# Optimization experiments

Measured on AMD Instinct MI355X. Metric: run time of the kernel, lower is better.

The kernel has to match this reference:

```python
import jax, jax.numpy as jnp
import numpy as np

B, T, D, H = 4, 2048, 512, 8
DK = D // H

def setup_inputs() -> dict:
    key = jax.random.key(0)
    ks = jax.random.split(key, 5)
    s = 1.0 / np.sqrt(D)
    return {
        "x": jax.random.normal(ks[0], (B, T, D), dtype=jnp.float32),
        "Wq": jax.random.normal(ks[1], (D, D), dtype=jnp.float32) * s,
        "bq": jnp.zeros((D,), dtype=jnp.float32),
        "Wk": jax.random.normal(ks[2], (D, D), dtype=jnp.float32) * s,
        "bk": jnp.zeros((D,), dtype=jnp.float32),
        "Wv": jax.random.normal(ks[3], (D, D), dtype=jnp.float32) * s,
        "bv": jnp.zeros((D,), dtype=jnp.float32),
        "Wo": jax.random.normal(ks[4], (D, D), dtype=jnp.float32) * s,
        "bo": jnp.zeros((D,), dtype=jnp.float32),
    }

def reference(x, Wq, bq, Wk, bk, Wv, bv, Wo, bo):
    # Linear projections (torch Linear: x @ W.T + b); split into heads.
    q = (x @ Wq.T + bq).reshape(B, T, H, DK)  # [B,T,H,dk]
    k = (x @ Wk.T + bk).reshape(B, T, H, DK)
    v = (x @ Wv.T + bv).reshape(B, T, H, DK)
    scale = 1.0 / np.sqrt(DK)
    # scores: [B,H,T,T]
    scores = jnp.einsum("bqhd,bkhd->bhqk", q, k) * scale
    attn = jax.nn.softmax(scores, axis=-1)
    ctx = jnp.einsum("bhqk,bkhd->bqhd", attn, v).reshape(B, T, D)
    return ctx @ Wo.T + bo
```

## Files before the change

### kernel.cpp

```cpp
#include <hip/hip_runtime.h>
#include <stdint.h>

#define NB 4
#define NT 2048
#define ND 512
#define NH 8
#define NDK 64
#define NM (NB*NT)

typedef __attribute__((ext_vector_type(8))) short short8;
typedef __attribute__((ext_vector_type(4))) short bs4;
typedef __attribute__((ext_vector_type(4))) float f32x4;

__device__ __forceinline__ unsigned short f2b(float f) {
    union { float f; uint32_t u; } v; v.f = f;
    return (unsigned short)((v.u + 0x7FFFu + ((v.u >> 16) & 1u)) >> 16);
}

__device__ __forceinline__ void load_lds16(const void* g, void* l) {
    void* gn = const_cast<void*>(g);
    __builtin_amdgcn_global_load_lds((__attribute__((address_space(1))) void*)gn,
                                     (__attribute__((address_space(3))) void*)l,
                                     16, 0, 0);
}

__global__ void convert_all(const float* __restrict__ x,  const float* __restrict__ wq,
                            const float* __restrict__ wk, const float* __restrict__ wv,
                            const float* __restrict__ wo, unsigned short* __restrict__ dst) {
    size_t i = ((size_t)blockIdx.x * 256 + threadIdx.x) * 4;
    const float* src; size_t off;
    if (i < 4194304) { src = x; off = i; }
    else {
        size_t j = i - 4194304;
        src = (j < 262144) ? wq : (j < 524288) ? wk : (j < 786432) ? wv : wo;
        off = j & 262143;
    }
    f32x4 v = *(const f32x4*)(src + off);
    ushort4 r;
    r.x = f2b(v[0]); r.y = f2b(v[1]); r.z = f2b(v[2]); r.w = f2b(v[3]);
    *(ushort4*)(dst + i) = r;
}

__global__ __launch_bounds__(256, 3) void proj_gemm(
        const unsigned short* __restrict__ X,
        const unsigned short* __restrict__ Wbase,
        const float* __restrict__ bias0, const float* __restrict__ bias1,
        const float* __restrict__ bias2,
        unsigned short* __restrict__ Obase, unsigned short* __restrict__ VTb,
        float scale0) {
    const int z = blockIdx.z;
    const float* bias = (z == 0) ? bias0 : (z == 1 ? bias1 : bias2);
    const float scale = (z == 0) ? scale0 : 1.0f;

    int rowBase, colBase;
    const unsigned short *Ap, *Bp;
    if (z == 2) {
        rowBase = blockIdx.x * 128;  colBase = blockIdx.y * 128;
        Ap = Wbase + 2 * (ND * ND);  Bp = X;
    } else {
        rowBase = blockIdx.y * 128;  colBase = blockIdx.x * 128;
        Ap = X;                      Bp = Wbase + (size_t)z * (ND * ND);
    }

    __shared__ alignas(16) unsigned short ldsA[128 * 64];
    __shared__ alignas(16) unsigned short ldsW[128 * 64];

    const int tid = threadIdx.x;
    const int lane = tid & 63, wave = tid >> 6;
    const int quad = lane >> 4, l15 = lane & 15;
    const int wm = wave >> 1, wn = wave & 1;

    const int rS = tid >> 3;
    const int gc = (tid & 7) ^ (rS & 7);
    const unsigned short* gA = Ap + (size_t)(rowBase + rS) * ND + gc * 8;
    const unsigned short* gW = Bp + (size_t)(colBase + rS) * ND + gc * 8;
    const int ldst = wave * 512;

    const int swz = l15 & 7;

    f32x4 acc[4][4];
#pragma unroll
    for (int i = 0; i < 4; i++)
#pragma unroll
        for (int j = 0; j < 4; j++) acc[i][j] = (f32x4)0.0f;

    for (int kt = 0; kt < ND / 64; ++kt) {
        __syncthreads();
#pragma unroll
        for (int c = 0; c < 4; ++c) {
            load_lds16(gA + (size_t)c * 32 * ND, ldsA + c * 2048 + ldst);
            load_lds16(gW + (size_t)c * 32 * ND, ldsW + c * 2048 + ldst);
        }
        gA += 64; gW += 64;
        __syncthreads();

#pragma unroll
        for (int ks = 0; ks < 2; ++ks) {
            short8 af[4], bfm[4];
#pragma unroll
            for (int mt = 0; mt < 4; ++mt)
                af[mt] = *(const short8*)(ldsA + (wm * 64 + mt * 16 + l15) * 64
                                          + (((ks * 4 + quad) ^ swz) * 8));
#pragma unroll
            for (int nt = 0; nt < 4; ++nt)
                bfm[nt] = *(const short8*)(ldsW + (wn * 64 + nt * 16 + l15) * 64
                                           + (((ks * 4 + quad) ^ swz) * 8));
#pragma unroll
            for (int mt = 0; mt < 4; ++mt)
#pragma unroll
                for (int nt = 0; nt < 4; ++nt)
                    acc[mt][nt] = __builtin_amdgcn_mfma_f32_16x16x32_bf16(
                        af[mt], bfm[nt], acc[mt][nt], 0, 0, 0);
        }
    }

    if (z == 2) {
        const int bz = colBase >> 11;
        const int t0 = colBase & 2047;
        unsigned short* VTo = VTb + ((size_t)(bz * 512 + rowBase)) * NT + t0;
#pragma unroll
        for (int mt = 0; mt < 4; mt++)
#pragma unroll
            for (int reg = 0; reg < 4; reg++) {
                int m = wm * 64 + mt * 16 + quad * 4 + reg;
                float bm = bias[rowBase + m];
                unsigned short* dst = VTo + (size_t)m * NT + wn * 64 + l15;
#pragma unroll
                for (int nt = 0; nt < 4; nt++)
                    dst[nt * 16] = f2b(acc[mt][nt][reg] + bm);
            }
    } else {
        float biasr[4];
#pragma unroll
        for (int nt = 0; nt < 4; nt++)
            biasr[nt] = bias[colBase + wn * 64 + nt * 16 + l15];
        unsigned short* Oz = Obase + (size_t)z * ((size_t)NM * ND);
#pragma unroll
        for (int mt = 0; mt < 4; mt++) {
            int row = rowBase + wm * 64 + mt * 16 + quad * 4;
#pragma unroll
            for (int reg = 0; reg < 4; reg++) {
                unsigned short* dst = Oz + (size_t)(row + reg) * ND + colBase + wn * 64 + l15;
#pragma unroll
                for (int nt = 0; nt < 4; nt++)
                    dst[nt * 16] = f2b((acc[mt][nt][reg] + biasr[nt]) * scale);
            }
        }
    }
}

__global__ __launch_bounds__(256, 4) void out_gemm(
        const unsigned short* __restrict__ A, const unsigned short* __restrict__ W,
        const float* __restrict__ bias, float* __restrict__ OF) {
    __shared__ alignas(16) unsigned short ldsA[64 * 64];
    __shared__ alignas(16) unsigned short ldsW[128 * 64];

    const int tid = threadIdx.x;
    const int lane = tid & 63, wave = tid >> 6;
    const int quad = lane >> 4, l15 = lane & 15;
    const int wm = wave >> 1, wn = wave & 1;
    const int rowBase = blockIdx.y * 64;
    const int colBase = blockIdx.x * 128;

    const int rS = tid >> 3;
    const int gc = (tid & 7) ^ (rS & 7);
    const unsigned short* gA = A + (size_t)(rowBase + rS) * ND + gc * 8;
    const unsigned short* gW = W + (size_t)(colBase + rS) * ND + gc * 8;
    const int ldst = wave * 512;
    const int swz = l15 & 7;

    f32x4 acc[2][4];
#pragma unroll
    for (int mt = 0; mt < 2; mt++)
#pragma unroll
        for (int nt = 0; nt < 4; nt++) acc[mt][nt] = (f32x4)0.0f;

    for (int kt = 0; kt < ND / 64; ++kt) {
        __syncthreads();
#pragma unroll
        for (int c = 0; c < 2; ++c)
            load_lds16(gA + (size_t)c * 32 * ND, ldsA + c * 2048 + ldst);
#pragma unroll
        for (int c = 0; c < 4; ++c)
            load_lds16(gW + (size_t)c * 32 * ND, ldsW + c * 2048 + ldst);
        gA += 64; gW += 64;
        __syncthreads();

#pragma unroll
        for (int ks = 0; ks < 2; ++ks) {
            short8 af[2], bfm[4];
#pragma unroll
            for (int mt = 0; mt < 2; ++mt)
                af[mt] = *(const short8*)(ldsA + (wm * 32 + mt * 16 + l15) * 64
                                          + (((ks * 4 + quad) ^ swz) * 8));
#pragma unroll
            for (int nt = 0; nt < 4; ++nt)
                bfm[nt] = *(const short8*)(ldsW + (wn * 64 + nt * 16 + l15) * 64
                                           + (((ks * 4 + quad) ^ swz) * 8));
#pragma unroll
            for (int mt = 0; mt < 2; ++mt)
#pragma unroll
                for (int nt = 0; nt < 4; ++nt)
                    acc[mt][nt] = __builtin_amdgcn_mfma_f32_16x16x32_bf16(
                        af[mt], bfm[nt], acc[mt][nt], 0, 0, 0);
        }
    }

    float biasr[4];
#pragma unroll
    for (int nt = 0; nt < 4; nt++)
        biasr[nt] = bias[colBase + wn * 64 + nt * 16 + l15];

#pragma unroll
    for (int mt = 0; mt < 2; mt++)
#pragma unroll
        for (int reg = 0; reg < 4; reg++) {
            int row = rowBase + wm * 32 + mt * 16 + quad * 4 + reg;
            float* dst = OF + (size_t)row * ND + colBase + wn * 64 + l15;
#pragma unroll
            for (int nt = 0; nt < 4; nt++)
                dst[nt * 16] = acc[mt][nt][reg] + biasr[nt];
        }
}

__global__ __launch_bounds__(256, 4) void attn_kernel(
        const unsigned short* __restrict__ Qb, const unsigned short* __restrict__ Kb,
        const unsigned short* __restrict__ VTb, unsigned short* __restrict__ Cb) {
    const int qt = blockIdx.x, h = blockIdx.y, b = blockIdx.z;
    __shared__ alignas(16) unsigned short Ks[128 * 64];
    __shared__ alignas(16) unsigned short Vt[64 * 128];

    const int tid = threadIdx.x, lane = tid & 63, wave = tid >> 6;
    const int quad = lane >> 4, l15 = lane & 15;
    const size_t headOff = (size_t)h * NDK;
    const size_t rowB = (size_t)b * NT;
    const unsigned short* VT = VTb + (size_t)(b * NH + h) * ((size_t)NDK * NT);

    short8 aq[2];
#pragma unroll
    for (int ks = 0; ks < 2; ++ks)
        aq[ks] = *(const short8*)(Qb + (rowB + qt * 64 + wave * 16 + l15) * ND
                                  + headOff + ks * 32 + quad * 8);

    const int rK = tid >> 3;
    const int gK8 = (tid & 7) ^ (rK & 7);
    const unsigned short* gK = Kb + (rowB + rK) * ND + headOff + gK8 * 8;
    const int rV = tid >> 4;
    const int gV8 = (tid & 15) ^ (rV & 7);
    const unsigned short* gV = VT + (size_t)rV * NT + gV8 * 8;
    const int ldst = wave * 512;

    const int swz = l15 & 7;
    const int qh = quad >> 1, qlo = quad & 1;
    const unsigned short* kb0 = Ks + l15 * 64 + ((quad ^ swz) * 8);
    const unsigned short* kb1 = Ks + l15 * 64 + (((4 + quad) ^ swz) * 8);
    const unsigned short* vbp[4];
#pragma unroll
    for (int k2 = 0; k2 < 4; ++k2)
        vbp[k2] = Vt + l15 * 128 + (((k2 * 2 + qh) ^ swz) * 8) + qlo * 4;

    f32x4 o[4];
#pragma unroll
    for (int nt = 0; nt < 4; nt++) o[nt] = (f32x4)0.0f;
    float lacc = 0.0f;

    for (int kv = 0; kv < NT / 128; ++kv) {
        __syncthreads();
#pragma unroll
        for (int c = 0; c < 4; ++c) {
            load_lds16(gK + (size_t)c * 32 * ND, Ks + c * 2048 + ldst);
            load_lds16(gV + (size_t)c * 16 * NT, Vt + c * 2048 + ldst);
        }
        gK += 128 * ND; gV += 128;
        __syncthreads();

#pragma unroll
        for (int kt = 0; kt < 8; ++kt) {
            f32x4 st = (f32x4)0.0f;
            st = __builtin_amdgcn_mfma_f32_16x16x32_bf16(
                *(const short8*)(kb0 + kt * 1024), aq[0], st, 0, 0, 0);
            st = __builtin_amdgcn_mfma_f32_16x16x32_bf16(
                *(const short8*)(kb1 + kt * 1024), aq[1], st, 0, 0, 0);
            float p0 = exp2f(st[0]), p1 = exp2f(st[1]);
            float p2 = exp2f(st[2]), p3 = exp2f(st[3]);
            lacc += (p0 + p1) + (p2 + p3);
            uint32_t lo = __builtin_amdgcn_perm(__float_as_uint(p1), __float_as_uint(p0),
                                                0x07060302u);
            uint32_t hi = __builtin_amdgcn_perm(__float_as_uint(p3), __float_as_uint(p2),
                                                0x07060302u);
            union { uint32_t w[2]; bs4 v; } cvt;
            cvt.w[0] = lo; cvt.w[1] = hi;
            const unsigned short* vb = vbp[kt & 3] + (kt >> 2) * 64;
#pragma unroll
            for (int nt = 0; nt < 4; ++nt)
                o[nt] = __builtin_amdgcn_mfma_f32_16x16x16bf16_1k(
                    cvt.v, *(const bs4*)(vb + nt * 2048), o[nt], 0, 0, 0);
        }
    }

    lacc += __shfl_xor(lacc, 16);
    lacc += __shfl_xor(lacc, 32);

#pragma unroll
    for (int reg = 0; reg < 4; ++reg) {
        float inv = 1.0f / __shfl(lacc, quad * 4 + reg);
        size_t row = rowB + qt * 64 + wave * 16 + quad * 4 + reg;
#pragma unroll
        for (int nt = 0; nt < 4; ++nt)
            Cb[row * ND + headOff + nt * 16 + l15] = f2b(o[nt][reg] * inv);
    }
}

extern "C" void kernel_launch(void* const* d_in, const int* in_sizes, int n_in,
                              void* d_out, int out_size, void* d_ws, size_t ws_size,
                              hipStream_t stream) {
    (void)in_sizes; (void)n_in; (void)out_size; (void)ws_size;
    const float* x  = (const float*)d_in[0];
    const float* Wq = (const float*)d_in[1];
    const float* bq = (const float*)d_in[2];
    const float* Wk = (const float*)d_in[3];
    const float* bk = (const float*)d_in[4];
    const float* Wv = (const float*)d_in[5];
    const float* bv = (const float*)d_in[6];
    const float* Wo = (const float*)d_in[7];
    const float* bo = (const float*)d_in[8];
    float* out = (float*)d_out;

    unsigned short* ws  = (unsigned short*)d_ws;
    unsigned short* xb  = ws;
    unsigned short* wqb = xb + 4194304;
    unsigned short* Qb  = wqb + 4 * 262144;
    unsigned short* Kb  = Qb + 4194304;
    unsigned short* VTb = Kb + 4194304;
    unsigned short* Cb  = VTb + 4194304;
    unsigned short* wob = wqb + 3 * 262144;

    convert_all<<<5120, 256, 0, stream>>>(x, Wq, Wk, Wv, Wo, ws);

    const float qscale = 0.125f * 1.44269504f;
    proj_gemm<<<dim3(4, 64, 3), 256, 0, stream>>>(xb, wqb, bq, bk, bv, Qb, VTb, qscale);
    attn_kernel<<<dim3(32, 8, 4), 256, 0, stream>>>(Qb, Kb, VTb, Cb);
    out_gemm<<<dim3(4, 128), 256, 0, stream>>>(Cb, wob, bo, out);
}
```

Before: 174.4 us.

## Double-buffer K/V tiles, 128-row query tiles, wider MFMA in attention

Result: no change. 172.9 us (-0.9%).

```diff
diff --git a/kernel.cpp b/kernel.cpp
--- a/kernel.cpp
+++ b/kernel.cpp
@@ -9,7 +9,6 @@
 #define NM (NB*NT)
 
 typedef __attribute__((ext_vector_type(8))) short short8;
-typedef __attribute__((ext_vector_type(4))) short bs4;
 typedef __attribute__((ext_vector_type(4))) float f32x4;
 
 __device__ __forceinline__ unsigned short f2b(float f) {
@@ -223,12 +222,17 @@
         }
 }
 
-__global__ __launch_bounds__(256, 4) void attn_kernel(
+__global__ __launch_bounds__(256, 2) void attn_kernel(
         const unsigned short* __restrict__ Qb, const unsigned short* __restrict__ Kb,
         const unsigned short* __restrict__ VTb, unsigned short* __restrict__ Cb) {
-    const int qt = blockIdx.x, h = blockIdx.y, b = blockIdx.z;
-    __shared__ alignas(16) unsigned short Ks[128 * 64];
-    __shared__ alignas(16) unsigned short Vt[64 * 128];
+    const int L = blockIdx.x + 16 * (blockIdx.y + 8 * blockIdx.z);
+    const int s = L >> 3;
+    const int qt = s & 15;
+    const int g = (L & 7) + 8 * (s >> 4);
+    const int h = g & 7, b = g >> 3;
+
+    __shared__ alignas(16) unsigned short Ks[2 * 8192];
+    __shared__ alignas(16) unsigned short Vt[2 * 8192];
 
     const int tid = threadIdx.x, lane = tid & 63, wave = tid >> 6;
     const int quad = lane >> 4, l15 = lane & 15;
@@ -236,78 +240,108 @@
     const size_t rowB = (size_t)b * NT;
     const unsigned short* VT = VTb + (size_t)(b * NH + h) * ((size_t)NDK * NT);
 
-    short8 aq[2];
-#pragma unroll
-    for (int ks = 0; ks < 2; ++ks)
-        aq[ks] = *(const short8*)(Qb + (rowB + qt * 64 + wave * 16 + l15) * ND
-                                  + headOff + ks * 32 + quad * 8);
+    short8 aq[2][2];
+#pragma unroll
+    for (int t = 0; t < 2; ++t)
+#pragma unroll
+        for (int ks = 0; ks < 2; ++ks)
+            aq[t][ks] = *(const short8*)(Qb
+                + (rowB + qt * 128 + wave * 32 + t * 16 + l15) * ND
+                + headOff + ks * 32 + quad * 8);
 
     const int rK = tid >> 3;
+    const int kap = (rK < 16) ? ((rK >> 2) * 8 + (rK & 3))
+                              : (((rK - 16) >> 2) * 8 + 4 + ((rK - 16) & 3));
     const int gK8 = (tid & 7) ^ (rK & 7);
-    const unsigned short* gK = Kb + (rowB + rK) * ND + headOff + gK8 * 8;
+    const unsigned short* gK = Kb + (rowB + kap) * ND + headOff + gK8 * 8;
     const int rV = tid >> 4;
     const int gV8 = (tid & 15) ^ (rV & 7);
     const unsigned short* gV = VT + (size_t)rV * NT + gV8 * 8;
     const int ldst = wave * 512;
 
     const int swz = l15 & 7;
-    const int qh = quad >> 1, qlo = quad & 1;
-    const unsigned short* kb0 = Ks + l15 * 64 + ((quad ^ swz) * 8);
-    const unsigned short* kb1 = Ks + l15 * 64 + (((4 + quad) ^ swz) * 8);
-    const unsigned short* vbp[4];
-#pragma unroll
-    for (int k2 = 0; k2 < 4; ++k2)
-        vbp[k2] = Vt + l15 * 128 + (((k2 * 2 + qh) ^ swz) * 8) + qlo * 4;
-
-    f32x4 o[4];
-#pragma unroll
-    for (int nt = 0; nt < 4; nt++) o[nt] = (f32x4)0.0f;
-    float lacc = 0.0f;
-
-    for (int kv = 0; kv < NT / 128; ++kv) {
-        __syncthreads();
+    const int ko0 = l15 * 64 + ((quad ^ swz) * 8);
+    const int ko1 = l15 * 64 + (((4 + quad) ^ swz) * 8);
+
+    f32x4 o[2][4];
+#pragma unroll
+    for (int t = 0; t < 2; ++t)
+#pragma unroll
+        for (int nt = 0; nt < 4; ++nt) o[t][nt] = (f32x4)0.0f;
+    float lacc[2] = {0.0f, 0.0f};
+
+    auto STAGE = [&](int bb, int r) {
+        const unsigned short* k = gK + (size_t)r * 128 * ND;
+        const unsigned short* v = gV + (size_t)r * 128;
+        unsigned short* kd = Ks + bb * 8192 + ldst;
+        unsigned short* vd = Vt + bb * 8192 + ldst;
 #pragma unroll
         for (int c = 0; c < 4; ++c) {
-            load_lds16(gK + (size_t)c * 32 * ND, Ks + c * 2048 + ldst);
-            load_lds16(gV + (size_t)c * 16 * NT, Vt + c * 2048 + ldst);
-        }
-        gK += 128 * ND; gV += 128;
-        __syncthreads();
-
-#pragma unroll
-        for (int kt = 0; kt < 8; ++kt) {
-            f32x4 st = (f32x4)0.0f;
-            st = __builtin_amdgcn_mfma_f32_16x16x32_bf16(
-                *(const short8*)(kb0 + kt * 1024), aq[0], st, 0, 0, 0);
-            st = __builtin_amdgcn_mfma_f32_16x16x32_bf16(
-                *(const short8*)(kb1 + kt * 1024), aq[1], st, 0, 0, 0);
-            float p0 = exp2f(st[0]), p1 = exp2f(st[1]);
-            float p2 = exp2f(st[2]), p3 = exp2f(st[3]);
-            lacc += (p0 + p1) + (p2 + p3);
-            uint32_t lo = __builtin_amdgcn_perm(__float_as_uint(p1), __float_as_uint(p0),
-                                                0x07060302u);
-            uint32_t hi = __builtin_amdgcn_perm(__float_as_uint(p3), __float_as_uint(p2),
-                                                0x07060302u);
-            union { uint32_t w[2]; bs4 v; } cvt;
-            cvt.w[0] = lo; cvt.w[1] = hi;
-            const unsigned short* vb = vbp[kt & 3] + (kt >> 2) * 64;
+            load_lds16(k + (size_t)c * 32 * ND, kd + c * 2048);
+            load_lds16(v + (size_t)c * 16 * NT, vd + c * 2048);
+        }
+    };
+
+    STAGE(0, 0);
+    __syncthreads();
+
+    for (int kv = 0; kv < 16; ++kv) {
+        const int buf = kv & 1;
+        if (kv < 15) STAGE(buf ^ 1, kv + 1);
+
+        const unsigned short* KB = Ks + buf * 8192;
+        const unsigned short* VB = Vt + buf * 8192;
+#pragma unroll
+        for (int pb = 0; pb < 4; ++pb) {
+            short8 kA0 = *(const short8*)(KB + pb * 2048 + ko0);
+            short8 kA1 = *(const short8*)(KB + pb * 2048 + ko1);
+            short8 kB0 = *(const short8*)(KB + pb * 2048 + 1024 + ko0);
+            short8 kB1 = *(const short8*)(KB + pb * 2048 + 1024 + ko1);
+            const int vo = l15 * 128 + (((pb * 4 + quad) ^ swz) * 8);
+            short8 vf[4];
 #pragma unroll
             for (int nt = 0; nt < 4; ++nt)
-                o[nt] = __builtin_amdgcn_mfma_f32_16x16x16bf16_1k(
-                    cvt.v, *(const bs4*)(vb + nt * 2048), o[nt], 0, 0, 0);
-        }
-    }
-
-    lacc += __shfl_xor(lacc, 16);
-    lacc += __shfl_xor(lacc, 32);
-
-#pragma unroll
-    for (int reg = 0; reg < 4; ++reg) {
-        float inv = 1.0f / __shfl(lacc, quad * 4 + reg);
-        size_t row = rowB + qt * 64 + wave * 16 + quad * 4 + reg;
-#pragma unroll
-        for (int nt = 0; nt < 4; ++nt)
-            Cb[row * ND + headOff + nt * 16 + l15] = f2b(o[nt][reg] * inv);
+                vf[nt] = *(const short8*)(VB + vo + nt * 2048);
+
+#pragma unroll
+            for (int t = 0; t < 2; ++t) {
+                f32x4 sa = (f32x4)0.0f, sb = (f32x4)0.0f;
+                sa = __builtin_amdgcn_mfma_f32_16x16x32_bf16(kA0, aq[t][0], sa, 0, 0, 0);
+                sa = __builtin_amdgcn_mfma_f32_16x16x32_bf16(kA1, aq[t][1], sa, 0, 0, 0);
+                sb = __builtin_amdgcn_mfma_f32_16x16x32_bf16(kB0, aq[t][0], sb, 0, 0, 0);
+                sb = __builtin_amdgcn_mfma_f32_16x16x32_bf16(kB1, aq[t][1], sb, 0, 0, 0);
+                float pA0 = exp2f(sa[0]), pA1 = exp2f(sa[1]);
+                float pA2 = exp2f(sa[2]), pA3 = exp2f(sa[3]);
+                float pB0 = exp2f(sb[0]), pB1 = exp2f(sb[1]);
+                float pB2 = exp2f(sb[2]), pB3 = exp2f(sb[3]);
+                lacc[t] += ((pA0 + pA1) + (pA2 + pA3)) + ((pB0 + pB1) + (pB2 + pB3));
+                union { uint32_t w[4]; short8 v; } cv;
+                cv.w[0] = __builtin_amdgcn_perm(__float_as_uint(pA1), __float_as_uint(pA0), 0x07060302u);
+                cv.w[1] = __builtin_amdgcn_perm(__float_as_uint(pA3), __float_as_uint(pA2), 0x07060302u);
+                cv.w[2] = __builtin_amdgcn_perm(__float_as_uint(pB1), __float_as_uint(pB0), 0x07060302u);
+                cv.w[3] = __builtin_amdgcn_perm(__float_as_uint(pB3), __float_as_uint(pB2), 0x07060302u);
+#pragma unroll
+                for (int nt = 0; nt < 4; ++nt)
+                    o[t][nt] = __builtin_amdgcn_mfma_f32_16x16x32_bf16(
+                        cv.v, vf[nt], o[t][nt], 0, 0, 0);
+            }
+        }
+        __syncthreads();
+    }
+
+#pragma unroll
+    for (int t = 0; t < 2; ++t) {
+        float la = lacc[t];
+        la += __shfl_xor(la, 16);
+        la += __shfl_xor(la, 32);
+#pragma unroll
+        for (int reg = 0; reg < 4; ++reg) {
+            float inv = 1.0f / __shfl(la, quad * 4 + reg);
+            size_t row = rowB + qt * 128 + wave * 32 + t * 16 + quad * 4 + reg;
+#pragma unroll
+            for (int nt = 0; nt < 4; ++nt)
+                Cb[row * ND + headOff + nt * 16 + l15] = f2b(o[t][nt][reg] * inv);
+        }
     }
 }
 
@@ -339,6 +373,6 @@
 
     const float qscale = 0.125f * 1.44269504f;
     proj_gemm<<<dim3(4, 64, 3), 256, 0, stream>>>(xb, wqb, bq, bk, bv, Qb, VTb, qscale);
-    attn_kernel<<<dim3(32, 8, 4), 256, 0, stream>>>(Qb, Kb, VTb, Cb);
+    attn_kernel<<<dim3(16, 8, 4), 256, 0, stream>>>(Qb, Kb, VTb, Cb);
     out_gemm<<<dim3(4, 128), 256, 0, stream>>>(Cb, wob, bo, out);
 }
```
